# Optimization experiments

Measured on AMD Instinct MI355X. Metric: run time of the kernel, lower is better.

## Reference

```python
import jax, jax.numpy as jnp
import numpy as np

GRID = 64  # grid_size from init_kwargs
EPS = 1e-6

def setup_inputs() -> dict:
    key = jax.random.key(0)
    points = jax.random.normal(key, (16, 500000, 3), dtype=jnp.float32)
    return {"points": points}

def reference(points) -> jnp.ndarray:
    B, N, _ = points.shape
    G = GRID
    # per-batch min/max normalize to [-1, 1)
    pmin = points.min(axis=1, keepdims=True)  # [B,1,3]
    pmax = points.max(axis=1, keepdims=True)  # [B,1,3]
    norm = (points - pmin) / (pmax - pmin + EPS) * 2.0 - 1.0  # [B,N,3]
    # histogramdd over range [-1,1]^3 with G bins per dim:
    # bin width = 2/G; right edge inclusive -> clip index G to G-1
    in_range = jnp.all((norm >= -1.0) & (norm <= 1.0), axis=-1)  # [B,N]
    idx = jnp.clip(jnp.floor((norm + 1.0) * (0.5 * G)).astype(jnp.int32), 0, G - 1)  # [B,N,3]
    b_idx = jnp.arange(B, dtype=jnp.int32)[:, None]  # [B,1]
    flat = ((b_idx * G + idx[..., 0]) * G + idx[..., 1]) * G + idx[..., 2]  # [B,N]
    w = in_range.astype(points.dtype)
    counts = jnp.zeros((B * G * G * G,), dtype=points.dtype).at[flat.reshape(-1)].add(w.reshape(-1))
    return counts.reshape(B, 1, G, G, G)
```

## Files before the change

kernel.cpp:

```cpp
#include <hip/hip_runtime.h>

#define GRIDSZ 64
#define NBATCH 16
#define NPTS   500000
#define NTRIP  (NPTS / 4)
#define FLOATS_PER_BATCH (NPTS * 3)
#define BINS_PER_BATCH (GRIDSZ * GRIDSZ * GRIDSZ)

#define CHUNKS   32
#define HBLOCKS  (NBATCH * CHUNKS)
#define HTHREADS 512
#define R0  16
#define RSZ 32
#define WORDS8 (RSZ * RSZ * (RSZ / 4))

#define MMBLK 128
#define MMTOTTHREADS (MMBLK * NBATCH * 256)

#define FINAL_OFF 0
#define PART_OFF_U32 256
#define HIST_PART_OFF_U32 (PART_OFF_U32 + MMBLK * NBATCH * 8)

__global__ __launch_bounds__(256) void minmax_stage1(
        const float* __restrict__ pts, float* __restrict__ partials,
        float4* __restrict__ out4) {
    const int b = blockIdx.y;
    const int linBlk = b * MMBLK + blockIdx.x;
    const int linTid = linBlk * 256 + threadIdx.x;

    const float4 z = make_float4(0.f, 0.f, 0.f, 0.f);
    out4[linTid] = z;
    out4[linTid + MMTOTTHREADS] = z;

    const float4* __restrict__ p4 =
        reinterpret_cast<const float4*>(pts + (size_t)b * FLOATS_PER_BATCH);

    float mn[3] = {INFINITY, INFINITY, INFINITY};
    float mx[3] = {-INFINITY, -INFINITY, -INFINITY};

    const int stride = MMBLK * 256;
    for (int i = blockIdx.x * 256 + threadIdx.x; i < NTRIP; i += stride) {
        float4 A = p4[3 * i + 0];
        float4 B = p4[3 * i + 1];
        float4 C = p4[3 * i + 2];
        float xs[4] = {A.x, A.w, B.z, C.y};
        float ys[4] = {A.y, B.x, B.w, C.z};
        float zs[4] = {A.z, B.y, C.x, C.w};
#pragma unroll
        for (int j = 0; j < 4; ++j) {
            mn[0] = fminf(mn[0], xs[j]); mx[0] = fmaxf(mx[0], xs[j]);
            mn[1] = fminf(mn[1], ys[j]); mx[1] = fmaxf(mx[1], ys[j]);
            mn[2] = fminf(mn[2], zs[j]); mx[2] = fmaxf(mx[2], zs[j]);
        }
    }
#pragma unroll
    for (int m = 1; m < 64; m <<= 1) {
#pragma unroll
        for (int c = 0; c < 3; ++c) {
            mn[c] = fminf(mn[c], __shfl_xor(mn[c], m));
            mx[c] = fmaxf(mx[c], __shfl_xor(mx[c], m));
        }
    }
    __shared__ float red[4][6];
    const int wave = threadIdx.x >> 6;
    if ((threadIdx.x & 63) == 0) {
        red[wave][0] = mn[0]; red[wave][1] = mn[1]; red[wave][2] = mn[2];
        red[wave][3] = mx[0]; red[wave][4] = mx[1]; red[wave][5] = mx[2];
    }
    __syncthreads();
    if (threadIdx.x == 0) {
#pragma unroll
        for (int w = 1; w < 4; ++w) {
#pragma unroll
            for (int c = 0; c < 3; ++c) {
                red[0][c]     = fminf(red[0][c],     red[w][c]);
                red[0][3 + c] = fmaxf(red[0][3 + c], red[w][3 + c]);
            }
        }
        float4* slot = reinterpret_cast<float4*>(partials + (size_t)linBlk * 8);
        slot[0] = make_float4(red[0][0], red[0][1], red[0][2], red[0][3]);
        slot[1] = make_float4(red[0][4], red[0][5], 0.0f, 0.0f);
    }
}

__global__ __launch_bounds__(MMBLK) void minmax_stage2(
        const float* __restrict__ partials, float* __restrict__ finals) {
    const int b = blockIdx.x;
    const float4* slot = reinterpret_cast<const float4*>(
        partials + (size_t)(b * MMBLK + threadIdx.x) * 8);
    float4 a = slot[0];
    float4 c = slot[1];
    float mn[3] = {a.x, a.y, a.z};
    float mx[3] = {a.w, c.x, c.y};
#pragma unroll
    for (int m = 1; m < 64; m <<= 1) {
#pragma unroll
        for (int k = 0; k < 3; ++k) {
            mn[k] = fminf(mn[k], __shfl_xor(mn[k], m));
            mx[k] = fmaxf(mx[k], __shfl_xor(mx[k], m));
        }
    }
    __shared__ float red[2][6];
    const int wave = threadIdx.x >> 6;
    if ((threadIdx.x & 63) == 0) {
        red[wave][0] = mn[0]; red[wave][1] = mn[1]; red[wave][2] = mn[2];
        red[wave][3] = mx[0]; red[wave][4] = mx[1]; red[wave][5] = mx[2];
    }
    __syncthreads();
    if (threadIdx.x == 0) {
        float* f = finals + b * 8;
#pragma unroll
        for (int k = 0; k < 3; ++k) {
            float lo = fminf(red[0][k],     red[1][k]);
            float hi = fmaxf(red[0][3 + k], red[1][3 + k]);
            f[k]     = lo;
            f[3 + k] = (hi - lo) + 1e-6f;
        }
        f[6] = 0.0f; f[7] = 0.0f;
    }
}

__device__ __forceinline__ void bin_point(float x, float y, float z,
                                          float mn0, float mn1, float mn2,
                                          float d0, float d1, float d2,
                                          bool& ok, int& ix, int& iy, int& iz) {
    float tx = (x - mn0) / d0;
    float ty = (y - mn1) / d1;
    float tz = (z - mn2) / d2;
    float nx = tx * 2.0f - 1.0f;
    float ny = ty * 2.0f - 1.0f;
    float nz = tz * 2.0f - 1.0f;
    ok = (nx >= -1.0f) & (nx <= 1.0f) &
         (ny >= -1.0f) & (ny <= 1.0f) &
         (nz >= -1.0f) & (nz <= 1.0f);
    ix = (int)floorf((nx + 1.0f) * 32.0f);
    iy = (int)floorf((ny + 1.0f) * 32.0f);
    iz = (int)floorf((nz + 1.0f) * 32.0f);
    ix = min(max(ix, 0), GRIDSZ - 1);
    iy = min(max(iy, 0), GRIDSZ - 1);
    iz = min(max(iz, 0), GRIDSZ - 1);
}

__global__ __launch_bounds__(HTHREADS) void hist_lds_kernel(
        const float* __restrict__ pts, const float* __restrict__ mm_partials,
        unsigned* __restrict__ partials, float* __restrict__ out) {
    __shared__ unsigned cnt[WORDS8];
    __shared__ float fin[6];
    const int bx = blockIdx.x;
    const int b = bx >> 5;
    const int chunk = bx & (CHUNKS - 1);

    for (int w = threadIdx.x; w < WORDS8; w += HTHREADS) cnt[w] = 0u;

    if (threadIdx.x < MMBLK) {
        const float4* slot = reinterpret_cast<const float4*>(
            mm_partials + (size_t)(b * MMBLK + threadIdx.x) * 8);
        float4 a = slot[0];
        float4 c = slot[1];
        float mn[3] = {a.x, a.y, a.z};
        float mx[3] = {a.w, c.x, c.y};
#pragma unroll
        for (int m = 1; m < 64; m <<= 1) {
#pragma unroll
            for (int k = 0; k < 3; ++k) {
                mn[k] = fminf(mn[k], __shfl_xor(mn[k], m));
                mx[k] = fmaxf(mx[k], __shfl_xor(mx[k], m));
            }
        }
        __shared__ float red[2][6];
        const int wave = threadIdx.x >> 6;
        if ((threadIdx.x & 63) == 0) {
            red[wave][0] = mn[0]; red[wave][1] = mn[1]; red[wave][2] = mn[2];
            red[wave][3] = mx[0]; red[wave][4] = mx[1]; red[wave][5] = mx[2];
        }
        __syncthreads();
        if (threadIdx.x == 0) {
#pragma unroll
            for (int k = 0; k < 3; ++k) {
                float lo = fminf(red[0][k],     red[1][k]);
                float hi = fmaxf(red[0][3 + k], red[1][3 + k]);
                fin[k]     = lo;
                fin[3 + k] = (hi - lo) + 1e-6f;
            }
        }
    } else {
        __syncthreads();
    }
    __syncthreads();

    const float mn0 = fin[0], mn1 = fin[1], mn2 = fin[2];
    const float d0 = fin[3], d1 = fin[4], d2 = fin[5];

    const float4* __restrict__ p4 =
        reinterpret_cast<const float4*>(pts + (size_t)b * FLOATS_PER_BATCH);
    float* __restrict__ outb = out + (size_t)b * BINS_PER_BATCH;

    for (int i = chunk * HTHREADS + threadIdx.x; i < NTRIP; i += CHUNKS * HTHREADS) {
        float4 A = p4[3 * i + 0];
        float4 B = p4[3 * i + 1];
        float4 C = p4[3 * i + 2];
        float xs[4] = {A.x, A.w, B.z, C.y};
        float ys[4] = {A.y, B.x, B.w, C.z};
        float zs[4] = {A.z, B.y, C.x, C.w};
#pragma unroll
        for (int j = 0; j < 4; ++j) {
            bool ok; int ix, iy, iz;
            bin_point(xs[j], ys[j], zs[j], mn0, mn1, mn2, d0, d1, d2, ok, ix, iy, iz);
            if (ok) {
                unsigned rx = (unsigned)(ix - R0), ry = (unsigned)(iy - R0), rz = (unsigned)(iz - R0);
                if ((rx < RSZ) & (ry < RSZ) & (rz < RSZ)) {
                    unsigned word = (rx * RSZ + ry) * (RSZ / 4) + (rz >> 2);
                    atomicAdd(&cnt[word], 1u << ((rz & 3u) * 8u));
                } else {
                    int bin = (ix * GRIDSZ + iy) * GRIDSZ + iz;
                    atomicAdd(&outb[bin], 1.0f);
                }
            }
        }
    }
    __syncthreads();

    unsigned* __restrict__ slot = partials + (size_t)bx * WORDS8;
    for (int w = threadIdx.x; w < WORDS8; w += HTHREADS) slot[w] = cnt[w];
}

__global__ void reduce_kernel(const unsigned* __restrict__ partials,
                              float* __restrict__ out) {
    const int b = blockIdx.y;
    const int w = blockIdx.x * 256 + threadIdx.x;
    const unsigned* __restrict__ base = partials + (size_t)b * CHUNKS * WORDS8;
    unsigned s0 = 0, s1 = 0, s2 = 0, s3 = 0;
#pragma unroll 4
    for (int c = 0; c < CHUNKS; ++c) {
        unsigned v = base[(size_t)c * WORDS8 + w];
        s0 += v & 0xFFu;
        s1 += (v >> 8) & 0xFFu;
        s2 += (v >> 16) & 0xFFu;
        s3 += v >> 24;
    }
    int ix = R0 + (w >> 8);
    int iy = R0 + ((w >> 3) & (RSZ - 1));
    int iz = R0 + ((w & (RSZ / 4 - 1)) << 2);
    float* __restrict__ outb = out + (size_t)b * BINS_PER_BATCH;
    int bin = (ix * GRIDSZ + iy) * GRIDSZ + iz;
    *reinterpret_cast<float4*>(&outb[bin]) =
        make_float4((float)s0, (float)s1, (float)s2, (float)s3);
}

__global__ void hist_kernel(const float* __restrict__ pts,
                            const float* __restrict__ finals,
                            float* __restrict__ out) {
    const int b = blockIdx.y;
    const float mn0 = finals[b * 8 + 0], mn1 = finals[b * 8 + 1], mn2 = finals[b * 8 + 2];
    const float d0  = finals[b * 8 + 3], d1  = finals[b * 8 + 4], d2  = finals[b * 8 + 5];

    const float4* __restrict__ p4 =
        reinterpret_cast<const float4*>(pts + (size_t)b * FLOATS_PER_BATCH);
    float* __restrict__ outb = out + (size_t)b * BINS_PER_BATCH;

    const int stride = gridDim.x * blockDim.x;
    for (int i = blockIdx.x * blockDim.x + threadIdx.x; i < NTRIP; i += stride) {
        float4 A = p4[3 * i + 0];
        float4 B = p4[3 * i + 1];
        float4 C = p4[3 * i + 2];
        float xs[4] = {A.x, A.w, B.z, C.y};
        float ys[4] = {A.y, B.x, B.w, C.z};
        float zs[4] = {A.z, B.y, C.x, C.w};
#pragma unroll
        for (int j = 0; j < 4; ++j) {
            bool ok; int ix, iy, iz;
            bin_point(xs[j], ys[j], zs[j], mn0, mn1, mn2, d0, d1, d2, ok, ix, iy, iz);
            if (ok) {
                int bin = (ix * GRIDSZ + iy) * GRIDSZ + iz;
                atomicAdd(&outb[bin], 1.0f);
            }
        }
    }
}

extern "C" void kernel_launch(void* const* d_in, const int* in_sizes, int n_in,
                              void* d_out, int out_size, void* d_ws, size_t ws_size,
                              hipStream_t stream) {
    const float* pts = (const float*)d_in[0];
    float* out = (float*)d_out;
    unsigned* ws = (unsigned*)d_ws;

    float* finals = (float*)(ws + FINAL_OFF);
    float* mm_partials = (float*)(ws + PART_OFF_U32);
    unsigned* hist_partials = ws + HIST_PART_OFF_U32;

    const size_t need = ((size_t)HIST_PART_OFF_U32 + (size_t)HBLOCKS * WORDS8) * 4;

    minmax_stage1<<<dim3(MMBLK, NBATCH), 256, 0, stream>>>(
        pts, mm_partials, (float4*)out);

    if (ws_size >= need) {
        hist_lds_kernel<<<HBLOCKS, HTHREADS, 0, stream>>>(
            pts, mm_partials, hist_partials, out);
        reduce_kernel<<<dim3(WORDS8 / 256, NBATCH), 256, 0, stream>>>(
            hist_partials, out);
    } else {
        minmax_stage2<<<NBATCH, MMBLK, 0, stream>>>(mm_partials, finals);
        hist_kernel<<<dim3(128, NBATCH), 256, 0, stream>>>(pts, finals, out);
    }
}
```

Measured before the change: 64.23 us.

## Fuse minmax, histogram and reduce into one kernel with per-batch global barriers

Replaces the three-kernel sequence (minmax, LDS histogram, reduce) with a single persistent-style kernel. Per-batch spin barriers on global atomic counters synchronise the 32 chunk blocks of each batch between the minmax, histogram and reduction phases, and a tiny kernel resets the counters first. The aim is to cut launch gaps and the separate min/max pass. The spin barrier assumes all 512 blocks are co-resident, and any block that is not resident risks deadlock or stalls.

After: 180.5 us. +181.0%, slower.

```diff
diff --git a/kernel.cpp b/kernel.cpp
--- a/kernel.cpp
+++ b/kernel.cpp
@@ -8,116 +8,35 @@
 #define BINS_PER_BATCH (GRIDSZ * GRIDSZ * GRIDSZ)
 
 #define CHUNKS   32
-#define HBLOCKS  (NBATCH * CHUNKS)
-#define HTHREADS 512
+#define FBLOCKS  (NBATCH * CHUNKS)
+#define FTHREADS 512
 #define R0  16
 #define RSZ 32
 #define WORDS8 (RSZ * RSZ * (RSZ / 4))
 
 #define MMBLK 128
-#define MMTOTTHREADS (MMBLK * NBATCH * 256)
-
-#define FINAL_OFF 0
-#define PART_OFF_U32 256
-#define HIST_PART_OFF_U32 (PART_OFF_U32 + MMBLK * NBATCH * 8)
-
-__global__ __launch_bounds__(256) void minmax_stage1(
-        const float* __restrict__ pts, float* __restrict__ partials,
-        float4* __restrict__ out4) {
-    const int b = blockIdx.y;
-    const int linBlk = b * MMBLK + blockIdx.x;
-    const int linTid = linBlk * 256 + threadIdx.x;
-
-    const float4 z = make_float4(0.f, 0.f, 0.f, 0.f);
-    out4[linTid] = z;
-    out4[linTid + MMTOTTHREADS] = z;
-
-    const float4* __restrict__ p4 =
-        reinterpret_cast<const float4*>(pts + (size_t)b * FLOATS_PER_BATCH);
-
-    float mn[3] = {INFINITY, INFINITY, INFINITY};
-    float mx[3] = {-INFINITY, -INFINITY, -INFINITY};
-
-    const int stride = MMBLK * 256;
-    for (int i = blockIdx.x * 256 + threadIdx.x; i < NTRIP; i += stride) {
-        float4 A = p4[3 * i + 0];
-        float4 B = p4[3 * i + 1];
-        float4 C = p4[3 * i + 2];
-        float xs[4] = {A.x, A.w, B.z, C.y};
-        float ys[4] = {A.y, B.x, B.w, C.z};
-        float zs[4] = {A.z, B.y, C.x, C.w};
-#pragma unroll
-        for (int j = 0; j < 4; ++j) {
-            mn[0] = fminf(mn[0], xs[j]); mx[0] = fmaxf(mx[0], xs[j]);
-            mn[1] = fminf(mn[1], ys[j]); mx[1] = fmaxf(mx[1], ys[j]);
-            mn[2] = fminf(mn[2], zs[j]); mx[2] = fmaxf(mx[2], zs[j]);
-        }
-    }
-#pragma unroll
-    for (int m = 1; m < 64; m <<= 1) {
-#pragma unroll
-        for (int c = 0; c < 3; ++c) {
-            mn[c] = fminf(mn[c], __shfl_xor(mn[c], m));
-            mx[c] = fmaxf(mx[c], __shfl_xor(mx[c], m));
-        }
-    }
-    __shared__ float red[4][6];
-    const int wave = threadIdx.x >> 6;
-    if ((threadIdx.x & 63) == 0) {
-        red[wave][0] = mn[0]; red[wave][1] = mn[1]; red[wave][2] = mn[2];
-        red[wave][3] = mx[0]; red[wave][4] = mx[1]; red[wave][5] = mx[2];
-    }
+
+#define ARR1_OFF 0
+#define ARR2_OFF 16
+#define FINAL_OFF 128
+#define MMPART_OFF 256
+#define HPART_OFF (MMPART_OFF + 2048 * 8)
+
+__global__ void init_counters(unsigned* __restrict__ ws) {
+    if (threadIdx.x < 32) ws[threadIdx.x] = 0u;
+}
+
+__device__ __forceinline__ void batch_barrier(unsigned* cnt) {
     __syncthreads();
     if (threadIdx.x == 0) {
-#pragma unroll
-        for (int w = 1; w < 4; ++w) {
-#pragma unroll
-            for (int c = 0; c < 3; ++c) {
-                red[0][c]     = fminf(red[0][c],     red[w][c]);
-                red[0][3 + c] = fmaxf(red[0][3 + c], red[w][3 + c]);
-            }
-        }
-        float4* slot = reinterpret_cast<float4*>(partials + (size_t)linBlk * 8);
-        slot[0] = make_float4(red[0][0], red[0][1], red[0][2], red[0][3]);
-        slot[1] = make_float4(red[0][4], red[0][5], 0.0f, 0.0f);
-    }
-}
-
-__global__ __launch_bounds__(MMBLK) void minmax_stage2(
-        const float* __restrict__ partials, float* __restrict__ finals) {
-    const int b = blockIdx.x;
-    const float4* slot = reinterpret_cast<const float4*>(
-        partials + (size_t)(b * MMBLK + threadIdx.x) * 8);
-    float4 a = slot[0];
-    float4 c = slot[1];
-    float mn[3] = {a.x, a.y, a.z};
-    float mx[3] = {a.w, c.x, c.y};
-#pragma unroll
-    for (int m = 1; m < 64; m <<= 1) {
-#pragma unroll
-        for (int k = 0; k < 3; ++k) {
-            mn[k] = fminf(mn[k], __shfl_xor(mn[k], m));
-            mx[k] = fmaxf(mx[k], __shfl_xor(mx[k], m));
-        }
-    }
-    __shared__ float red[2][6];
-    const int wave = threadIdx.x >> 6;
-    if ((threadIdx.x & 63) == 0) {
-        red[wave][0] = mn[0]; red[wave][1] = mn[1]; red[wave][2] = mn[2];
-        red[wave][3] = mx[0]; red[wave][4] = mx[1]; red[wave][5] = mx[2];
-    }
-    __syncthreads();
-    if (threadIdx.x == 0) {
-        float* f = finals + b * 8;
-#pragma unroll
-        for (int k = 0; k < 3; ++k) {
-            float lo = fminf(red[0][k],     red[1][k]);
-            float hi = fmaxf(red[0][3 + k], red[1][3 + k]);
-            f[k]     = lo;
-            f[3 + k] = (hi - lo) + 1e-6f;
-        }
-        f[6] = 0.0f; f[7] = 0.0f;
-    }
+        __threadfence();
+        atomicAdd(cnt, 1u);
+        while (atomicAdd(cnt, 0u) < (unsigned)CHUNKS) {
+            __builtin_amdgcn_s_sleep(16);
+        }
+        __threadfence();
+    }
+    __syncthreads();
 }
 
 __device__ __forceinline__ void bin_point(float x, float y, float z,
@@ -141,61 +60,111 @@
     iz = min(max(iz, 0), GRIDSZ - 1);
 }
 
-__global__ __launch_bounds__(HTHREADS) void hist_lds_kernel(
-        const float* __restrict__ pts, const float* __restrict__ mm_partials,
-        unsigned* __restrict__ partials, float* __restrict__ out) {
+__global__ __launch_bounds__(FTHREADS, 4) void fused_kernel(
+        const float* __restrict__ pts,
+        float* __restrict__ mm_partials,
+        unsigned* __restrict__ hist_partials,
+        unsigned* __restrict__ arrive1,
+        unsigned* __restrict__ arrive2,
+        float* __restrict__ out) {
     __shared__ unsigned cnt[WORDS8];
+    __shared__ float red[8][6];
     __shared__ float fin[6];
+
     const int bx = blockIdx.x;
     const int b = bx >> 5;
     const int chunk = bx & (CHUNKS - 1);
-
-    for (int w = threadIdx.x; w < WORDS8; w += HTHREADS) cnt[w] = 0u;
-
-    if (threadIdx.x < MMBLK) {
+    const int tid = threadIdx.x;
+
+    for (int w = tid; w < WORDS8; w += FTHREADS) cnt[w] = 0u;
+
+    {
+        float4* outb4 = reinterpret_cast<float4*>(out + (size_t)b * BINS_PER_BATCH);
+        const float4 z = make_float4(0.f, 0.f, 0.f, 0.f);
+        const int base = chunk * 2048 + tid;
+#pragma unroll
+        for (int k = 0; k < 4; ++k) outb4[base + k * FTHREADS] = z;
+    }
+
+    const float4* __restrict__ p4 =
+        reinterpret_cast<const float4*>(pts + (size_t)b * FLOATS_PER_BATCH);
+
+    float mn[3] = {INFINITY, INFINITY, INFINITY};
+    float mx[3] = {-INFINITY, -INFINITY, -INFINITY};
+    for (int i = chunk * FTHREADS + tid; i < NTRIP; i += CHUNKS * FTHREADS) {
+        float4 A = p4[3 * i + 0];
+        float4 B = p4[3 * i + 1];
+        float4 C = p4[3 * i + 2];
+        float xs[4] = {A.x, A.w, B.z, C.y};
+        float ys[4] = {A.y, B.x, B.w, C.z};
+        float zs[4] = {A.z, B.y, C.x, C.w};
+#pragma unroll
+        for (int j = 0; j < 4; ++j) {
+            mn[0] = fminf(mn[0], xs[j]); mx[0] = fmaxf(mx[0], xs[j]);
+            mn[1] = fminf(mn[1], ys[j]); mx[1] = fmaxf(mx[1], ys[j]);
+            mn[2] = fminf(mn[2], zs[j]); mx[2] = fmaxf(mx[2], zs[j]);
+        }
+    }
+#pragma unroll
+    for (int m = 1; m < 64; m <<= 1) {
+#pragma unroll
+        for (int c = 0; c < 3; ++c) {
+            mn[c] = fminf(mn[c], __shfl_xor(mn[c], m));
+            mx[c] = fmaxf(mx[c], __shfl_xor(mx[c], m));
+        }
+    }
+    const int wave = tid >> 6;
+    if ((tid & 63) == 0) {
+        red[wave][0] = mn[0]; red[wave][1] = mn[1]; red[wave][2] = mn[2];
+        red[wave][3] = mx[0]; red[wave][4] = mx[1]; red[wave][5] = mx[2];
+    }
+    __syncthreads();
+    if (tid == 0) {
+#pragma unroll
+        for (int w = 1; w < 8; ++w) {
+#pragma unroll
+            for (int c = 0; c < 3; ++c) {
+                red[0][c]     = fminf(red[0][c],     red[w][c]);
+                red[0][3 + c] = fmaxf(red[0][3 + c], red[w][3 + c]);
+            }
+        }
+        float4* slot = reinterpret_cast<float4*>(mm_partials + (size_t)bx * 8);
+        slot[0] = make_float4(red[0][0], red[0][1], red[0][2], red[0][3]);
+        slot[1] = make_float4(red[0][4], red[0][5], 0.0f, 0.0f);
+    }
+
+    batch_barrier(&arrive1[b]);
+
+    if (tid < CHUNKS) {
         const float4* slot = reinterpret_cast<const float4*>(
-            mm_partials + (size_t)(b * MMBLK + threadIdx.x) * 8);
+            mm_partials + (size_t)(b * CHUNKS + tid) * 8);
         float4 a = slot[0];
         float4 c = slot[1];
-        float mn[3] = {a.x, a.y, a.z};
-        float mx[3] = {a.w, c.x, c.y};
-#pragma unroll
-        for (int m = 1; m < 64; m <<= 1) {
+        float pmn[3] = {a.x, a.y, a.z};
+        float pmx[3] = {a.w, c.x, c.y};
+#pragma unroll
+        for (int m = 1; m < 32; m <<= 1) {
 #pragma unroll
             for (int k = 0; k < 3; ++k) {
-                mn[k] = fminf(mn[k], __shfl_xor(mn[k], m));
-                mx[k] = fmaxf(mx[k], __shfl_xor(mx[k], m));
-            }
-        }
-        __shared__ float red[2][6];
-        const int wave = threadIdx.x >> 6;
-        if ((threadIdx.x & 63) == 0) {
-            red[wave][0] = mn[0]; red[wave][1] = mn[1]; red[wave][2] = mn[2];
-            red[wave][3] = mx[0]; red[wave][4] = mx[1]; red[wave][5] = mx[2];
-        }
-        __syncthreads();
-        if (threadIdx.x == 0) {
+                pmn[k] = fminf(pmn[k], __shfl_xor(pmn[k], m));
+                pmx[k] = fmaxf(pmx[k], __shfl_xor(pmx[k], m));
+            }
+        }
+        if (tid == 0) {
 #pragma unroll
             for (int k = 0; k < 3; ++k) {
-                float lo = fminf(red[0][k],     red[1][k]);
-                float hi = fmaxf(red[0][3 + k], red[1][3 + k]);
-                fin[k]     = lo;
-                fin[3 + k] = (hi - lo) + 1e-6f;
-            }
-        }
-    } else {
-        __syncthreads();
+                fin[k]     = pmn[k];
+                fin[3 + k] = (pmx[k] - pmn[k]) + 1e-6f;
+            }
+        }
     }
     __syncthreads();
 
     const float mn0 = fin[0], mn1 = fin[1], mn2 = fin[2];
     const float d0 = fin[3], d1 = fin[4], d2 = fin[5];
-
-    const float4* __restrict__ p4 =
-        reinterpret_cast<const float4*>(pts + (size_t)b * FLOATS_PER_BATCH);
     float* __restrict__ outb = out + (size_t)b * BINS_PER_BATCH;
 
-    for (int i = chunk * HTHREADS + threadIdx.x; i < NTRIP; i += CHUNKS * HTHREADS) {
+    for (int i = chunk * FTHREADS + tid; i < NTRIP; i += CHUNKS * FTHREADS) {
         float4 A = p4[3 * i + 0];
         float4 B = p4[3 * i + 1];
         float4 C = p4[3 * i + 2];
@@ -220,31 +189,128 @@
     }
     __syncthreads();
 
-    unsigned* __restrict__ slot = partials + (size_t)bx * WORDS8;
-    for (int w = threadIdx.x; w < WORDS8; w += HTHREADS) slot[w] = cnt[w];
-}
-
-__global__ void reduce_kernel(const unsigned* __restrict__ partials,
-                              float* __restrict__ out) {
+    {
+        unsigned* __restrict__ slot = hist_partials + (size_t)bx * WORDS8;
+        for (int w = tid; w < WORDS8; w += FTHREADS) slot[w] = cnt[w];
+    }
+
+    batch_barrier(&arrive2[b]);
+
+    if (tid < 256) {
+        const int w = chunk * 256 + tid;
+        const unsigned* __restrict__ base =
+            hist_partials + (size_t)b * CHUNKS * WORDS8;
+        unsigned s0 = 0, s1 = 0, s2 = 0, s3 = 0;
+#pragma unroll 4
+        for (int c = 0; c < CHUNKS; ++c) {
+            unsigned v = base[(size_t)c * WORDS8 + w];
+            s0 += v & 0xFFu;
+            s1 += (v >> 8) & 0xFFu;
+            s2 += (v >> 16) & 0xFFu;
+            s3 += v >> 24;
+        }
+        int ry = (w >> 3) & (RSZ - 1);
+        int rz = (w & (RSZ / 4 - 1)) << 2;
+        int bin = ((R0 + chunk) * GRIDSZ + (R0 + ry)) * GRIDSZ + (R0 + rz);
+        *reinterpret_cast<float4*>(&outb[bin]) =
+            make_float4((float)s0, (float)s1, (float)s2, (float)s3);
+    }
+}
+
+__global__ __launch_bounds__(256) void minmax_stage1(
+        const float* __restrict__ pts, float* __restrict__ partials,
+        float4* __restrict__ out4) {
     const int b = blockIdx.y;
-    const int w = blockIdx.x * 256 + threadIdx.x;
-    const unsigned* __restrict__ base = partials + (size_t)b * CHUNKS * WORDS8;
-    unsigned s0 = 0, s1 = 0, s2 = 0, s3 = 0;
-#pragma unroll 4
-    for (int c = 0; c < CHUNKS; ++c) {
-        unsigned v = base[(size_t)c * WORDS8 + w];
-        s0 += v & 0xFFu;
-        s1 += (v >> 8) & 0xFFu;
-        s2 += (v >> 16) & 0xFFu;
-        s3 += v >> 24;
-    }
-    int ix = R0 + (w >> 8);
-    int iy = R0 + ((w >> 3) & (RSZ - 1));
-    int iz = R0 + ((w & (RSZ / 4 - 1)) << 2);
-    float* __restrict__ outb = out + (size_t)b * BINS_PER_BATCH;
-    int bin = (ix * GRIDSZ + iy) * GRIDSZ + iz;
-    *reinterpret_cast<float4*>(&outb[bin]) =
-        make_float4((float)s0, (float)s1, (float)s2, (float)s3);
+    const int linBlk = b * MMBLK + blockIdx.x;
+    const int linTid = linBlk * 256 + threadIdx.x;
+    const float4 z = make_float4(0.f, 0.f, 0.f, 0.f);
+    out4[linTid] = z;
+    out4[linTid + MMBLK * NBATCH * 256] = z;
+
+    const float4* __restrict__ p4 =
+        reinterpret_cast<const float4*>(pts + (size_t)b * FLOATS_PER_BATCH);
+    float mn[3] = {INFINITY, INFINITY, INFINITY};
+    float mx[3] = {-INFINITY, -INFINITY, -INFINITY};
+    const int stride = MMBLK * 256;
+    for (int i = blockIdx.x * 256 + threadIdx.x; i < NTRIP; i += stride) {
+        float4 A = p4[3 * i + 0];
+        float4 B = p4[3 * i + 1];
+        float4 C = p4[3 * i + 2];
+        float xs[4] = {A.x, A.w, B.z, C.y};
+        float ys[4] = {A.y, B.x, B.w, C.z};
+        float zs[4] = {A.z, B.y, C.x, C.w};
+#pragma unroll
+        for (int j = 0; j < 4; ++j) {
+            mn[0] = fminf(mn[0], xs[j]); mx[0] = fmaxf(mx[0], xs[j]);
+            mn[1] = fminf(mn[1], ys[j]); mx[1] = fmaxf(mx[1], ys[j]);
+            mn[2] = fminf(mn[2], zs[j]); mx[2] = fmaxf(mx[2], zs[j]);
+        }
+    }
+#pragma unroll
+    for (int m = 1; m < 64; m <<= 1) {
+#pragma unroll
+        for (int c = 0; c < 3; ++c) {
+            mn[c] = fminf(mn[c], __shfl_xor(mn[c], m));
+            mx[c] = fmaxf(mx[c], __shfl_xor(mx[c], m));
+        }
+    }
+    __shared__ float red[4][6];
+    const int wave = threadIdx.x >> 6;
+    if ((threadIdx.x & 63) == 0) {
+        red[wave][0] = mn[0]; red[wave][1] = mn[1]; red[wave][2] = mn[2];
+        red[wave][3] = mx[0]; red[wave][4] = mx[1]; red[wave][5] = mx[2];
+    }
+    __syncthreads();
+    if (threadIdx.x == 0) {
+#pragma unroll
+        for (int w = 1; w < 4; ++w) {
+#pragma unroll
+            for (int c = 0; c < 3; ++c) {
+                red[0][c]     = fminf(red[0][c],     red[w][c]);
+                red[0][3 + c] = fmaxf(red[0][3 + c], red[w][3 + c]);
+            }
+        }
+        float4* slot = reinterpret_cast<float4*>(partials + (size_t)linBlk * 8);
+        slot[0] = make_float4(red[0][0], red[0][1], red[0][2], red[0][3]);
+        slot[1] = make_float4(red[0][4], red[0][5], 0.0f, 0.0f);
+    }
+}
+
+__global__ __launch_bounds__(MMBLK) void minmax_stage2(
+        const float* __restrict__ partials, float* __restrict__ finals) {
+    const int b = blockIdx.x;
+    const float4* slot = reinterpret_cast<const float4*>(
+        partials + (size_t)(b * MMBLK + threadIdx.x) * 8);
+    float4 a = slot[0];
+    float4 c = slot[1];
+    float mn[3] = {a.x, a.y, a.z};
+    float mx[3] = {a.w, c.x, c.y};
+#pragma unroll
+    for (int m = 1; m < 64; m <<= 1) {
+#pragma unroll
+        for (int k = 0; k < 3; ++k) {
+            mn[k] = fminf(mn[k], __shfl_xor(mn[k], m));
+            mx[k] = fmaxf(mx[k], __shfl_xor(mx[k], m));
+        }
+    }
+    __shared__ float red[2][6];
+    const int wave = threadIdx.x >> 6;
+    if ((threadIdx.x & 63) == 0) {
+        red[wave][0] = mn[0]; red[wave][1] = mn[1]; red[wave][2] = mn[2];
+        red[wave][3] = mx[0]; red[wave][4] = mx[1]; red[wave][5] = mx[2];
+    }
+    __syncthreads();
+    if (threadIdx.x == 0) {
+        float* f = finals + b * 8;
+#pragma unroll
+        for (int k = 0; k < 3; ++k) {
+            float lo = fminf(red[0][k],     red[1][k]);
+            float hi = fmaxf(red[0][3 + k], red[1][3 + k]);
+            f[k]     = lo;
+            f[3 + k] = (hi - lo) + 1e-6f;
+        }
+        f[6] = 0.0f; f[7] = 0.0f;
+    }
 }
 
 __global__ void hist_kernel(const float* __restrict__ pts,
@@ -253,11 +319,9 @@
     const int b = blockIdx.y;
     const float mn0 = finals[b * 8 + 0], mn1 = finals[b * 8 + 1], mn2 = finals[b * 8 + 2];
     const float d0  = finals[b * 8 + 3], d1  = finals[b * 8 + 4], d2  = finals[b * 8 + 5];
-
     const float4* __restrict__ p4 =
         reinterpret_cast<const float4*>(pts + (size_t)b * FLOATS_PER_BATCH);
     float* __restrict__ outb = out + (size_t)b * BINS_PER_BATCH;
-
     const int stride = gridDim.x * blockDim.x;
     for (int i = blockIdx.x * blockDim.x + threadIdx.x; i < NTRIP; i += stride) {
         float4 A = p4[3 * i + 0];
@@ -286,20 +350,19 @@
     unsigned* ws = (unsigned*)d_ws;
 
     float* finals = (float*)(ws + FINAL_OFF);
-    float* mm_partials = (float*)(ws + PART_OFF_U32);
-    unsigned* hist_partials = ws + HIST_PART_OFF_U32;
-
-    const size_t need = ((size_t)HIST_PART_OFF_U32 + (size_t)HBLOCKS * WORDS8) * 4;
-
-    minmax_stage1<<<dim3(MMBLK, NBATCH), 256, 0, stream>>>(
-        pts, mm_partials, (float4*)out);
+    float* mm_partials = (float*)(ws + MMPART_OFF);
+    unsigned* hist_partials = ws + HPART_OFF;
+
+    const size_t need = ((size_t)HPART_OFF + (size_t)FBLOCKS * WORDS8) * 4;
 
     if (ws_size >= need) {
-        hist_lds_kernel<<<HBLOCKS, HTHREADS, 0, stream>>>(
-            pts, mm_partials, hist_partials, out);
-        reduce_kernel<<<dim3(WORDS8 / 256, NBATCH), 256, 0, stream>>>(
-            hist_partials, out);
+        init_counters<<<1, 64, 0, stream>>>(ws);
+        fused_kernel<<<FBLOCKS, FTHREADS, 0, stream>>>(
+            pts, mm_partials, hist_partials,
+            ws + ARR1_OFF, ws + ARR2_OFF, out);
     } else {
+        minmax_stage1<<<dim3(MMBLK, NBATCH), 256, 0, stream>>>(
+            pts, mm_partials, (float4*)out);
         minmax_stage2<<<NBATCH, MMBLK, 0, stream>>>(mm_partials, finals);
         hist_kernel<<<dim3(128, NBATCH), 256, 0, stream>>>(pts, finals, out);
     }
```

## Fuse partial-histogram reduction into histogram kernel via last-block counter

Applied to the files above, without the earlier changes.

Removes the separate reduce kernel launch. Each histogram block writes its packed byte-count partial, fences, and bumps a per-batch done counter; the last block of each batch sums all 32 partials and writes the central region to the output. The counter is reset in the minmax kernel. This saves one launch and its gap, but the final reduction now runs on only 16 blocks (one per batch), which serializes work that was spread across many blocks before.

New measurement: 213.9 us. 3.33x slower.

```diff
diff --git a/kernel.cpp b/kernel.cpp
--- a/kernel.cpp
+++ b/kernel.cpp
@@ -17,16 +17,19 @@
 #define MMBLK 128
 #define MMTOTTHREADS (MMBLK * NBATCH * 256)
 
-#define FINAL_OFF 0
+#define DONE_OFF 0
+#define FINAL_OFF 128
 #define PART_OFF_U32 256
 #define HIST_PART_OFF_U32 (PART_OFF_U32 + MMBLK * NBATCH * 8)
 
 __global__ __launch_bounds__(256) void minmax_stage1(
         const float* __restrict__ pts, float* __restrict__ partials,
-        float4* __restrict__ out4) {
+        unsigned* __restrict__ done, float4* __restrict__ out4) {
     const int b = blockIdx.y;
     const int linBlk = b * MMBLK + blockIdx.x;
     const int linTid = linBlk * 256 + threadIdx.x;
+
+    if (blockIdx.x == 0 && threadIdx.x == 0) done[b] = 0u;
 
     const float4 z = make_float4(0.f, 0.f, 0.f, 0.f);
     out4[linTid] = z;
@@ -143,9 +146,11 @@
 
 __global__ __launch_bounds__(HTHREADS) void hist_lds_kernel(
         const float* __restrict__ pts, const float* __restrict__ mm_partials,
-        unsigned* __restrict__ partials, float* __restrict__ out) {
+        unsigned* __restrict__ partials, unsigned* __restrict__ done,
+        float* __restrict__ out) {
     __shared__ unsigned cnt[WORDS8];
     __shared__ float fin[6];
+    __shared__ int isLast;
     const int bx = blockIdx.x;
     const int b = bx >> 5;
     const int chunk = bx & (CHUNKS - 1);
@@ -220,31 +225,40 @@
     }
     __syncthreads();
 
-    unsigned* __restrict__ slot = partials + (size_t)bx * WORDS8;
-    for (int w = threadIdx.x; w < WORDS8; w += HTHREADS) slot[w] = cnt[w];
-}
-
-__global__ void reduce_kernel(const unsigned* __restrict__ partials,
-                              float* __restrict__ out) {
-    const int b = blockIdx.y;
-    const int w = blockIdx.x * 256 + threadIdx.x;
-    const unsigned* __restrict__ base = partials + (size_t)b * CHUNKS * WORDS8;
-    unsigned s0 = 0, s1 = 0, s2 = 0, s3 = 0;
+    {
+        unsigned* __restrict__ slot = partials + (size_t)bx * WORDS8;
+        for (int w = threadIdx.x; w < WORDS8; w += HTHREADS) slot[w] = cnt[w];
+    }
+
+    __threadfence();
+    __syncthreads();
+    if (threadIdx.x == 0) {
+        unsigned old = atomicAdd(&done[b], 1u);
+        isLast = (old == (unsigned)(CHUNKS - 1)) ? 1 : 0;
+    }
+    __syncthreads();
+
+    if (isLast) {
+        __threadfence();
+        const unsigned* __restrict__ base = partials + (size_t)b * CHUNKS * WORDS8;
+        for (int w = threadIdx.x; w < WORDS8; w += HTHREADS) {
+            unsigned s0 = 0, s1 = 0, s2 = 0, s3 = 0;
 #pragma unroll 4
-    for (int c = 0; c < CHUNKS; ++c) {
-        unsigned v = base[(size_t)c * WORDS8 + w];
-        s0 += v & 0xFFu;
-        s1 += (v >> 8) & 0xFFu;
-        s2 += (v >> 16) & 0xFFu;
-        s3 += v >> 24;
-    }
-    int ix = R0 + (w >> 8);
-    int iy = R0 + ((w >> 3) & (RSZ - 1));
-    int iz = R0 + ((w & (RSZ / 4 - 1)) << 2);
-    float* __restrict__ outb = out + (size_t)b * BINS_PER_BATCH;
-    int bin = (ix * GRIDSZ + iy) * GRIDSZ + iz;
-    *reinterpret_cast<float4*>(&outb[bin]) =
-        make_float4((float)s0, (float)s1, (float)s2, (float)s3);
+            for (int c = 0; c < CHUNKS; ++c) {
+                unsigned v = base[(size_t)c * WORDS8 + w];
+                s0 += v & 0xFFu;
+                s1 += (v >> 8) & 0xFFu;
+                s2 += (v >> 16) & 0xFFu;
+                s3 += v >> 24;
+            }
+            int ix = R0 + (w >> 8);
+            int iy = R0 + ((w >> 3) & (RSZ - 1));
+            int iz = R0 + ((w & (RSZ / 4 - 1)) << 2);
+            int bin = (ix * GRIDSZ + iy) * GRIDSZ + iz;
+            *reinterpret_cast<float4*>(&outb[bin]) =
+                make_float4((float)s0, (float)s1, (float)s2, (float)s3);
+        }
+    }
 }
 
 __global__ void hist_kernel(const float* __restrict__ pts,
@@ -288,17 +302,16 @@
     float* finals = (float*)(ws + FINAL_OFF);
     float* mm_partials = (float*)(ws + PART_OFF_U32);
     unsigned* hist_partials = ws + HIST_PART_OFF_U32;
+    unsigned* done = ws + DONE_OFF;
 
     const size_t need = ((size_t)HIST_PART_OFF_U32 + (size_t)HBLOCKS * WORDS8) * 4;
 
     minmax_stage1<<<dim3(MMBLK, NBATCH), 256, 0, stream>>>(
-        pts, mm_partials, (float4*)out);
+        pts, mm_partials, done, (float4*)out);
 
     if (ws_size >= need) {
         hist_lds_kernel<<<HBLOCKS, HTHREADS, 0, stream>>>(
-            pts, mm_partials, hist_partials, out);
-        reduce_kernel<<<dim3(WORDS8 / 256, NBATCH), 256, 0, stream>>>(
-            hist_partials, out);
+            pts, mm_partials, hist_partials, done, out);
     } else {
         minmax_stage2<<<NBATCH, MMBLK, 0, stream>>>(mm_partials, finals);
         hist_kernel<<<dim3(128, NBATCH), 256, 0, stream>>>(pts, finals, out);
```
